# Kernel tuning notes

Hardware: AMD Instinct MI355X
Metric: run time of the kernel (lower is better)

Reference implementation:

```python
import jax, jax.numpy as jnp
import numpy as np

N = 50000       # nodes
E = 800000      # edges (avg degree 16)
H = 64          # hidden_channels
T = 4           # towers
F = H // T      # per-tower channels (divide_input=True) = 16
NAGG, NSC = 5, 3
# degree histogram passed as mol_deg -> avg log-degree scaler constant (as in PyG PNAConv)
MOL_DEG = np.array([0, 5, 15, 30, 25, 15, 7, 2, 1], dtype=np.float64)
_bins = np.arange(len(MOL_DEG))
AVG_LOG = float((np.log(_bins + 1.0) * MOL_DEG).sum() / MOL_DEG.sum())


def setup_inputs() -> dict:
    key = jax.random.key(0)
    ks = jax.random.split(key, 12)
    g = lambda k, shp, s=0.1: jax.random.normal(k, shp, dtype=jnp.float32) * s
    return {
        "atom_x": g(ks[0], (N, H), 1.0),
        "bond_emb": g(ks[1], (5, H)),                      # Embedding(5, H)
        "edge_w": g(ks[2], (H, F)), "edge_b": jnp.zeros((F,), jnp.float32),
        "pre_w1": g(ks[3], (T, 3 * F, F)), "pre_b1": jnp.zeros((T, F), jnp.float32),
        "pre_w2": g(ks[4], (T, F, F)), "pre_b2": jnp.zeros((T, F), jnp.float32),
        "post_w1": g(ks[5], (T, (1 + NAGG * NSC) * F, F)), "post_b1": jnp.zeros((T, F), jnp.float32),
        "post_w2": g(ks[6], (T, F, F)), "post_b2": jnp.zeros((T, F), jnp.float32),
        "lin_w": g(ks[7], (H, H)), "lin_b": jnp.zeros((H,), jnp.float32),
        "ln_g": jnp.ones((H,), jnp.float32), "ln_b": jnp.zeros((H,), jnp.float32),
        "bond_x": jax.random.randint(ks[8], (E,), 0, 5),
        "atom_edge_index": jax.random.randint(ks[9], (2, E), 0, N),
    }


def reference(atom_x, bond_emb, edge_w, edge_b, pre_w1, pre_b1, pre_w2, pre_b2,
              post_w1, post_b1, post_w2, post_b2, lin_w, lin_b, ln_g, ln_b,
              bond_x, atom_edge_index):
    src, dst = atom_edge_index[0], atom_edge_index[1]
    # bond encoder + PNA edge encoder (edge_dim -> F_in)
    e = bond_emb[bond_x] @ edge_w + edge_b                       # [E, F]
    xt = atom_x.reshape(N, T, F)                                 # divide_input
    x_j, x_i = xt[src], xt[dst]                                  # [E, T, F]
    et = jnp.broadcast_to(e[:, None, :], (E, T, F))
    h = jnp.concatenate([x_i, x_j, et], axis=-1)                 # [E, T, 3F]
    # per-tower pre-MLP (Linear -> ReLU -> Linear)
    h = jax.nn.relu(jnp.einsum('etf,tfg->etg', h, pre_w1) + pre_b1)
    h = jnp.einsum('etf,tfg->etg', h, pre_w2) + pre_b2           # messages [E, T, F]

    s = jax.ops.segment_sum(h, dst, num_segments=N)
    cnt = jax.ops.segment_sum(jnp.ones((E,), h.dtype), dst, num_segments=N)
    cnt_c = jnp.maximum(cnt, 1.0)[:, None, None]
    mean = s / cnt_c
    mean2 = jax.ops.segment_sum(h * h, dst, num_segments=N) / cnt_c
    std = jnp.sqrt(jax.nn.relu(mean2 - mean * mean) + 1e-5)
    has = (cnt > 0)[:, None, None]
    mn = jnp.where(has, jax.ops.segment_min(h, dst, num_segments=N), 0.0)
    mx = jnp.where(has, jax.ops.segment_max(h, dst, num_segments=N), 0.0)
    agg = jnp.concatenate([s, mean, mn, mx, std], axis=-1)       # [N, T, 5F]

    # degree scalers (deg clamped to 1, as in PyG DegreeScalerAggregation)
    ld = jnp.log(jnp.maximum(cnt, 1.0) + 1.0)[:, None, None]
    agg = jnp.concatenate([agg, agg * (ld / AVG_LOG), agg * (AVG_LOG / ld)], axis=-1)  # [N, T, 15F]

    out = jnp.concatenate([xt, agg], axis=-1)                    # [N, T, 16F]
    # per-tower post-MLP, then mix towers with final Linear
    out = jax.nn.relu(jnp.einsum('ntf,tfg->ntg', out, post_w1) + post_b1)
    out = jnp.einsum('ntf,tfg->ntg', out, post_w2) + post_b2     # [N, T, F]
    out = out.reshape(N, H) @ lin_w + lin_b                      # [N, H]

    # LayerNorm + ReLU + residual (dropout is identity in eval)
    mu = out.mean(-1, keepdims=True)
    var = out.var(-1, keepdims=True)
    ln = (out - mu) / jnp.sqrt(var + 1e-5) * ln_g + ln_b
    return atom_x + jax.nn.relu(ln)
```

## Files before the change

### kernel.cpp

```cpp
#include <hip/hip_runtime.h>
#include <cstdint>

typedef unsigned short u16;

#define AVG_LOG_F 1.4862356961977451f
#define MAXD 64

#define OFF_W2   3072
#define OFF_PW1  4096
#define OFF_PW2  20480
#define OFF_LW   21504
#define OFF_PB1  25600
#define OFF_PB2  25664
#define OFF_QB1  25728
#define OFF_QB2  25792
#define OFF_LB   25856
#define OFF_LG   25920
#define OFF_LBN  25984
#define OFF_EWT  26128
#define IB       26448

__device__ __forceinline__ float bf2f(u16 u) {
    return __uint_as_float(((unsigned)u) << 16);
}
__device__ __forceinline__ u16 f2bf(float f) {
    unsigned u = __float_as_uint(f);
    u += 0x7fffu + ((u >> 16) & 1u);
    return (u16)(u >> 16);
}
__device__ __forceinline__ float rdin(const void* p, long j, int mode) {
    if (mode == 0) return bf2f(((const u16*)p)[j]);
    return ((const float*)p)[j];
}
template <int MODE>
__device__ __forceinline__ void load16c(const void* p, long base, float* o) {
    if (MODE == 0) {
        const u16* q = (const u16*)p + base;
        uint4 a = *(const uint4*)q;
        uint4 b = *(const uint4*)(q + 8);
        o[0]  = __uint_as_float(a.x << 16); o[1]  = __uint_as_float(a.x & 0xffff0000u);
        o[2]  = __uint_as_float(a.y << 16); o[3]  = __uint_as_float(a.y & 0xffff0000u);
        o[4]  = __uint_as_float(a.z << 16); o[5]  = __uint_as_float(a.z & 0xffff0000u);
        o[6]  = __uint_as_float(a.w << 16); o[7]  = __uint_as_float(a.w & 0xffff0000u);
        o[8]  = __uint_as_float(b.x << 16); o[9]  = __uint_as_float(b.x & 0xffff0000u);
        o[10] = __uint_as_float(b.y << 16); o[11] = __uint_as_float(b.y & 0xffff0000u);
        o[12] = __uint_as_float(b.z << 16); o[13] = __uint_as_float(b.z & 0xffff0000u);
        o[14] = __uint_as_float(b.w << 16); o[15] = __uint_as_float(b.w & 0xffff0000u);
    } else {
        const float* q = (const float*)p + base;
        float4 a = *(const float4*)q;
        float4 b = *(const float4*)(q + 4);
        float4 c = *(const float4*)(q + 8);
        float4 d = *(const float4*)(q + 12);
        o[0]=a.x; o[1]=a.y; o[2]=a.z; o[3]=a.w;
        o[4]=b.x; o[5]=b.y; o[6]=b.z; o[7]=b.w;
        o[8]=c.x; o[9]=c.y; o[10]=c.z; o[11]=c.w;
        o[12]=d.x; o[13]=d.y; o[14]=d.z; o[15]=d.w;
    }
}

template <int MODE>
__device__ __forceinline__ void y_loop(const void* ax, const void* pre_w1, float* wsY, float* wsXW,
                                       int Nn, int wave, int nwaves, int l) {
    const int t = l >> 4, g = l & 15;
    float wxi[16], wxj[16];
#pragma unroll
    for (int f = 0; f < 16; f++) {
        wxi[f] = rdin(pre_w1, t * 768 + f * 16 + g, MODE);
        wxj[f] = rdin(pre_w1, t * 768 + (16 + f) * 16 + g, MODE);
    }
    for (int n = wave; n < Nn; n += nwaves) {
        float xj[16];
        load16c<MODE>(ax, (long)n * 64 + t * 16, xj);
        float accY = 0.f, accX = 0.f;
#pragma unroll
        for (int f = 0; f < 16; f++) {
            accY = fmaf(xj[f], wxj[f], accY);
            accX = fmaf(xj[f], wxi[f], accX);
        }
        wsY[(long)n * 64 + l]  = accY;
        wsXW[(long)n * 64 + l] = accX;
    }
}

__global__ __launch_bounds__(256) void k_prep(
    const int* __restrict__ dstp, const int* __restrict__ srcp, const int* __restrict__ bondp,
    const void* bond_emb, const void* edge_w, const void* edge_b,
    const void* pre_w1, const void* pre_b1, const void* pre_w2, const void* pre_b2,
    const void* post_w1, const void* post_b1, const void* post_w2, const void* post_b2,
    const void* lin_w, const void* lin_b, const void* ln_g, const void* ln_b,
    const void* ax, float* wsf, float* wsY, float* wsXW,
    int* __restrict__ cnt, int* __restrict__ pk, int* modep,
    int Nn, int E, int NIB)
{
    int tid = threadIdx.x;
    if ((int)blockIdx.x >= NIB) {
        int e = ((int)blockIdx.x - NIB) * 256 + tid;
        if (e < E) {
            int d = dstp[e];
            int pos = atomicAdd(&cnt[d], 1);
            if (pos < MAXD) pk[d * MAXD + pos] = (srcp[e] << 9) | (bondp[e] & 7);
        }
        return;
    }
    __shared__ int csh;
    __shared__ float ET[80];
    if (tid == 0) csh = 0;
    __syncthreads();
    {
        unsigned v = ((const unsigned*)ax)[tid];
        unsigned lo = v & 0xffffu;
        int ee = (int)((lo >> 7) & 0xff);
        int isbf = (lo == 0u) || (ee >= 110 && ee <= 140);
        atomicAdd(&csh, isbf);
    }
    __syncthreads();
    int mode = (csh >= 192) ? 0 : 1;

    int b = (int)blockIdx.x;
    int gt = b * 256 + tid;
    int gs = NIB * 256;
    if (b == 0 && tid == 0) modep[0] = mode;

    for (int j = gt; j < 1024; j += gs)  wsf[OFF_W2 + j]  = rdin(pre_w2, j, mode);
    for (int j = gt; j < 16384; j += gs) wsf[OFF_PW1 + j] = rdin(post_w1, j, mode);
    for (int j = gt; j < 1024; j += gs)  wsf[OFF_PW2 + j] = rdin(post_w2, j, mode);
    for (int j = gt; j < 4096; j += gs)  wsf[OFF_LW + j]  = rdin(lin_w, j, mode);
    for (int j = gt; j < 64; j += gs) {
        wsf[OFF_PB1 + j] = rdin(pre_b1, j, mode);
        wsf[OFF_PB2 + j] = rdin(pre_b2, j, mode);
        wsf[OFF_QB1 + j] = rdin(post_b1, j, mode);
        wsf[OFF_QB2 + j] = rdin(post_b2, j, mode);
        wsf[OFF_LB + j]  = rdin(lin_b, j, mode);
        wsf[OFF_LG + j]  = rdin(ln_g, j, mode);
        wsf[OFF_LBN + j] = rdin(ln_b, j, mode);
    }
    if (b == 0) {
        if (tid < 80) {
            int bb = tid >> 4, f = tid & 15;
            float acc = rdin(edge_b, f, mode);
            for (int k = 0; k < 64; k++)
                acc = fmaf(rdin(bond_emb, bb * 64 + k, mode), rdin(edge_w, k * 16 + f, mode), acc);
            ET[tid] = acc;
        }
        __syncthreads();
        for (int j = tid; j < 320; j += 256) {
            int bb = j >> 6, ll = j & 63, tt = ll >> 4, gg = ll & 15;
            float acc = rdin(pre_b1, tt * 16 + gg, mode);
#pragma unroll
            for (int f = 0; f < 16; f++)
                acc = fmaf(ET[bb * 16 + f], rdin(pre_w1, tt * 768 + (32 + f) * 16 + gg, mode), acc);
            wsf[OFF_EWT + j] = acc;
        }
    }
    int wave = gt >> 6;
    int nwaves = gs >> 6;
    int l = tid & 63;
    if (mode == 0) y_loop<0>(ax, pre_w1, wsY, wsXW, Nn, wave, nwaves, l);
    else           y_loop<1>(ax, pre_w1, wsY, wsXW, Nn, wave, nwaves, l);
}

__global__ __launch_bounds__(256, 4) void k_node(
    const void* __restrict__ ax, const float* __restrict__ Yp, const float* __restrict__ XWp,
    const int* __restrict__ pk, const int* __restrict__ cnt,
    const float* __restrict__ wsf, void* __restrict__ outp,
    const int* __restrict__ modep, int Nn)
{
    __shared__ float hb[4][8][64];
    __shared__ float zws[4][5][64];
    __shared__ float qp[4][4][64];
    __shared__ float xrow[4][64];
    __shared__ float scl1s[4], scl2s[4];
    const int w = threadIdx.x >> 6;
    const int l = threadIdx.x & 63;
    const int t = l >> 4;
    const int g = l & 15;
    const int n = blockIdx.x * 4 + w;
    const int mode = modep[0];
    const bool active = (n < Nn);
    const int nn = active ? n : 0;

    const float* W2  = wsf + OFF_W2  + t * 256;
    const float* PW1 = wsf + OFF_PW1 + t * 4096;
    const float* PW2 = wsf + OFF_PW2 + t * 256;

    int probe = __builtin_amdgcn_update_dpp(0, l & 15, 0x121, 0xf, 0xf, false);
    int p0 = __builtin_amdgcn_readfirstlane(probe);
    const int dir = (p0 == 1) ? 1 : -1;

    float w2r[16];
#pragma unroll
    for (int r = 0; r < 16; r++) w2r[r] = W2[((g + dir * r) & 15) * 16 + g];

    float pb2g = wsf[OFF_PB2 + t * 16 + g];
    float qb1g = wsf[OFF_QB1 + t * 16 + g];
    float qb2g = wsf[OFF_QB2 + t * 16 + g];

    int deg = active ? cnt[nn] : 0;
    if (deg > MAXD) deg = MAXD;

    int   pkvAll = pk[nn * MAXD + l];
    float XWv    = XWp[(long)nn * 64 + l];
    zws[w][0][l] = XWv + wsf[OFF_EWT + 0 * 64 + l];
    zws[w][1][l] = XWv + wsf[OFF_EWT + 1 * 64 + l];
    zws[w][2][l] = XWv + wsf[OFF_EWT + 2 * 64 + l];
    zws[w][3][l] = XWv + wsf[OFF_EWT + 3 * 64 + l];
    zws[w][4][l] = XWv + wsf[OFF_EWT + 4 * 64 + l];
    xrow[w][l]   = rdin(ax, (long)nn * 64 + l, mode);

    float s = 0.f, s2 = 0.f, mn = 3.0e38f, mx = -3.0e38f;

#define ROTFMA(r, ctrl)                                                              \
    {                                                                                \
        int tmp_ = __builtin_amdgcn_update_dpp(0, hi, ctrl, 0xf, 0xf, false);        \
        float hv_ = __int_as_float(tmp_);                                            \
        if ((r) & 1) mb = fmaf(hv_, w2r[r], mb);                                     \
        else         ma = fmaf(hv_, w2r[r], ma);                                     \
    }

    for (int kb = 0; kb < deg; kb += 8) {
        float yv[8];
        int   vs[8];
#pragma unroll
        for (int k = 0; k < 8; k++) {
            if (kb + k < deg) {
                vs[k] = __builtin_amdgcn_readlane(pkvAll, kb + k);
                yv[k] = Yp[(vs[k] >> 3) + l];
            }
        }
#pragma unroll
        for (int k = 0; k < 8; k++) {
            if (kb + k < deg) {
                float h = fmaxf(yv[k] + zws[w][vs[k] & 7][l], 0.f);
                int hi = __float_as_uint(h);
                float ma = fmaf(h, w2r[0], pb2g);
                float mb = 0.f;
                ROTFMA(1, 0x121);  ROTFMA(2, 0x122);  ROTFMA(3, 0x123);
                ROTFMA(4, 0x124);  ROTFMA(5, 0x125);  ROTFMA(6, 0x126);
                ROTFMA(7, 0x127);  ROTFMA(8, 0x128);  ROTFMA(9, 0x129);
                ROTFMA(10, 0x12A); ROTFMA(11, 0x12B); ROTFMA(12, 0x12C);
                ROTFMA(13, 0x12D); ROTFMA(14, 0x12E); ROTFMA(15, 0x12F);
                float m = ma + mb;
                s += m;
                s2 = fmaf(m, m, s2);
                mn = fminf(mn, m);
                mx = fmaxf(mx, m);
            }
        }
    }
#undef ROTFMA

    if (deg == 0) { mn = 0.f; mx = 0.f; }
    float cf = (float)(deg > 0 ? deg : 1);
    float inv = 1.0f / cf;
    float mean = s * inv;
    float var = s2 * inv - mean * mean;
    float sd = sqrtf(fmaxf(var, 0.f) + 1e-5f);
    float ldv = logf(cf + 1.0f);
    float sc1 = ldv * (1.0f / AVG_LOG_F);
    float sc2 = AVG_LOG_F / ldv;

    hb[w][0][l] = s;
    hb[w][1][l] = mean;
    hb[w][2][l] = mn;
    hb[w][3][l] = mx;
    hb[w][4][l] = sd;
    if (l == 0) { scl1s[w] = sc1; scl2s[w] = sc2; }
    __syncthreads();

    const int F0 = w * 4;
    float q0[4] = {0,0,0,0}, q1[4] = {0,0,0,0}, q2[4] = {0,0,0,0};
    {
        float xa[4][4];
#pragma unroll
        for (int nd = 0; nd < 4; nd++) {
            float4 v = *(const float4*)&xrow[nd][t * 16 + F0];
            xa[nd][0] = v.x; xa[nd][1] = v.y; xa[nd][2] = v.z; xa[nd][3] = v.w;
        }
#pragma unroll
        for (int fi = 0; fi < 4; fi++) {
            float wv = PW1[(F0 + fi) * 16 + g];
#pragma unroll
            for (int nd = 0; nd < 4; nd++) q0[nd] = fmaf(xa[nd][fi], wv, q0[nd]);
        }
    }
#pragma unroll
    for (int a = 0; a < 5; a++) {
        float xa[4][4];
#pragma unroll
        for (int nd = 0; nd < 4; nd++) {
            float4 v = *(const float4*)&hb[nd][a][t * 16 + F0];
            xa[nd][0] = v.x; xa[nd][1] = v.y; xa[nd][2] = v.z; xa[nd][3] = v.w;
        }
        const int rb = 16 + a * 16;
#pragma unroll
        for (int fi = 0; fi < 4; fi++) {
            const int r = (rb + F0 + fi) * 16 + g;
            float w0  = PW1[r];
            float w1  = PW1[r + 80 * 16];
            float w2v = PW1[r + 160 * 16];
#pragma unroll
            for (int nd = 0; nd < 4; nd++) {
                float x = xa[nd][fi];
                q0[nd] = fmaf(x, w0,  q0[nd]);
                q1[nd] = fmaf(x, w1,  q1[nd]);
                q2[nd] = fmaf(x, w2v, q2[nd]);
            }
        }
    }
#pragma unroll
    for (int nd = 0; nd < 4; nd++)
        qp[w][nd][l] = fmaf(scl2s[nd], q2[nd], fmaf(scl1s[nd], q1[nd], q0[nd]));
    __syncthreads();

    {
        float q0s = qp[0][w][l] + qp[1][w][l] + qp[2][w][l] + qp[3][w][l];
        float p1 = fmaxf(q0s + qb1g, 0.f);
        hb[w][5][l] = p1;
        float pw2c[16];
#pragma unroll
        for (int f = 0; f < 16; f++) pw2c[f] = PW2[f * 16 + g];
        float m2 = qb2g;
        const float4* pp = (const float4*)&hb[w][5][t * 16];
        float4 p0v = pp[0], r1 = pp[1], r2 = pp[2], r3 = pp[3];
        m2 = fmaf(p0v.x, pw2c[0],  m2); m2 = fmaf(p0v.y, pw2c[1],  m2);
        m2 = fmaf(p0v.z, pw2c[2],  m2); m2 = fmaf(p0v.w, pw2c[3],  m2);
        m2 = fmaf(r1.x, pw2c[4],  m2); m2 = fmaf(r1.y, pw2c[5],  m2);
        m2 = fmaf(r1.z, pw2c[6],  m2); m2 = fmaf(r1.w, pw2c[7],  m2);
        m2 = fmaf(r2.x, pw2c[8],  m2); m2 = fmaf(r2.y, pw2c[9],  m2);
        m2 = fmaf(r2.z, pw2c[10], m2); m2 = fmaf(r2.w, pw2c[11], m2);
        m2 = fmaf(r3.x, pw2c[12], m2); m2 = fmaf(r3.y, pw2c[13], m2);
        m2 = fmaf(r3.z, pw2c[14], m2); m2 = fmaf(r3.w, pw2c[15], m2);
        hb[w][6][l] = m2;
    }
    __syncthreads();

    {
        const float* LW = wsf + OFF_LW;
        const int fb = w * 16;
        float lw[4] = {0,0,0,0};
#pragma unroll
        for (int c = 0; c < 4; c++) {
            float pa[4][4];
#pragma unroll
            for (int nd = 0; nd < 4; nd++) {
                float4 v = *(const float4*)&hb[nd][6][fb + 4 * c];
                pa[nd][0] = v.x; pa[nd][1] = v.y; pa[nd][2] = v.z; pa[nd][3] = v.w;
            }
#pragma unroll
            for (int fi = 0; fi < 4; fi++) {
                float wl = LW[(fb + 4 * c + fi) * 64 + l];
#pragma unroll
                for (int nd = 0; nd < 4; nd++) lw[nd] = fmaf(pa[nd][fi], wl, lw[nd]);
            }
        }
#pragma unroll
        for (int nd = 0; nd < 4; nd++) qp[w][nd][l] = lw[nd];
    }
    __syncthreads();

    {
        float a = wsf[OFF_LB + l] + qp[0][w][l] + qp[1][w][l] + qp[2][w][l] + qp[3][w][l];
        float s1 = a, sq = a * a;
#pragma unroll
        for (int o = 1; o < 64; o <<= 1) { s1 += __shfl_xor(s1, o); sq += __shfl_xor(sq, o); }
        float mu = s1 * (1.0f / 64.0f);
        float varl = sq * (1.0f / 64.0f) - mu * mu;
        float ln = (a - mu) * rsqrtf(varl + 1e-5f) * wsf[OFF_LG + l] + wsf[OFF_LBN + l];
        if (active) {
            long idx = (long)n * 64 + l;
            float res = xrow[w][l] + fmaxf(ln, 0.f);
            if (mode == 0) ((u16*)outp)[idx] = f2bf(res);
            else           ((float*)outp)[idx] = res;
        }
    }
}

extern "C" void kernel_launch(void* const* d_in, const int* in_sizes, int n_in,
                              void* d_out, int out_size, void* d_ws, size_t ws_size,
                              hipStream_t stream) {
    const void* atom_x   = d_in[0];
    const void* bond_emb = d_in[1];
    const void* edge_w   = d_in[2];
    const void* edge_b   = d_in[3];
    const void* pre_w1   = d_in[4];
    const void* pre_b1   = d_in[5];
    const void* pre_w2   = d_in[6];
    const void* pre_b2   = d_in[7];
    const void* post_w1  = d_in[8];
    const void* post_b1  = d_in[9];
    const void* post_w2  = d_in[10];
    const void* post_b2  = d_in[11];
    const void* lin_w    = d_in[12];
    const void* lin_b    = d_in[13];
    const void* ln_g     = d_in[14];
    const void* ln_b     = d_in[15];
    const int* bond_x    = (const int*)d_in[16];
    const int* aei       = (const int*)d_in[17];

    int E  = in_sizes[16];
    int Nn = in_sizes[0] / 64;
    const int* srcp = aei;
    const int* dstp = aei + E;

    float* wsf = (float*)d_ws;
    int*   wsi = (int*)d_ws;

    size_t o = IB;
    int* modep = wsi + o; o += 16;
    int* cnt   = wsi + o; o += Nn;
    o = (o + 63) & ~(size_t)63;
    int* pk    = wsi + o; o += (size_t)Nn * MAXD;
    float* Yp  = (float*)(wsi + o); o += (size_t)Nn * 64;
    float* XWp = (float*)(wsi + o); o += (size_t)Nn * 64;

    const int NIB  = 1600;
    const int SBLK = (E + 255) / 256;

    (void)hipMemsetAsync(cnt, 0, (size_t)Nn * sizeof(int), stream);
    k_prep<<<NIB + SBLK, 256, 0, stream>>>(dstp, srcp, bond_x,
                                           bond_emb, edge_w, edge_b,
                                           pre_w1, pre_b1, pre_w2, pre_b2,
                                           post_w1, post_b1, post_w2, post_b2,
                                           lin_w, lin_b, ln_g, ln_b,
                                           atom_x, wsf, Yp, XWp, cnt, pk, modep, Nn, E, NIB);
    dim3 gn((Nn + 3) / 4, 1, 1);
    k_node<<<gn, 256, 0, stream>>>(atom_x, Yp, XWp, pk, cnt, wsf, d_out, modep, Nn);
}
```

Baseline: 298.9 us.

## Compute per-edge pre-MLP second layer with fp16 MFMA over 16-edge batches

Replaces the per-edge DPP-rotation FMA matvec for the second pre-MLP layer with 16x16x16 fp16 MFMA instructions. Each wave stages 16 edges of hidden activations as fp16 in a swizzled shared buffer and multiplies them against per-tower W2 fragments. Per-lane partial statistics are then reduced across lane groups with shuffles. This cuts the VALU/DPP instruction count per edge but adds shared-memory round trips, padding waste for nodes with low degree, and fp16 precision loss.

```diff
diff --git a/kernel.cpp b/kernel.cpp
--- a/kernel.cpp
+++ b/kernel.cpp
@@ -2,6 +2,8 @@
 #include <cstdint>
 
 typedef unsigned short u16;
+typedef _Float16 half4v __attribute__((ext_vector_type(4)));
+typedef float f32x4 __attribute__((ext_vector_type(4)));
 
 #define AVG_LOG_F 1.4862356961977451f
 #define MAXD 64
@@ -167,6 +169,7 @@
     const int* __restrict__ modep, int Nn)
 {
     __shared__ float hb[4][8][64];
+    __shared__ _Float16 hbh[4][16][64];
     __shared__ float zws[4][5][64];
     __shared__ float qp[4][4][64];
     __shared__ float xrow[4][64];
@@ -180,19 +183,23 @@
     const bool active = (n < Nn);
     const int nn = active ? n : 0;
 
-    const float* W2  = wsf + OFF_W2  + t * 256;
     const float* PW1 = wsf + OFF_PW1 + t * 4096;
     const float* PW2 = wsf + OFF_PW2 + t * 256;
 
-    int probe = __builtin_amdgcn_update_dpp(0, l & 15, 0x121, 0xf, 0xf, false);
-    int p0 = __builtin_amdgcn_readfirstlane(probe);
-    const int dir = (p0 == 1) ? 1 : -1;
-
-    float w2r[16];
-#pragma unroll
-    for (int r = 0; r < 16; r++) w2r[r] = W2[((g + dir * r) & 15) * 16 + g];
-
-    float pb2g = wsf[OFF_PB2 + t * 16 + g];
+    half4v bfr[4];
+    float pb2a[4];
+    {
+        const int k4 = (l >> 4) << 2;
+#pragma unroll
+        for (int tt = 0; tt < 4; tt++) {
+            half4v bv;
+#pragma unroll
+            for (int i = 0; i < 4; i++)
+                bv[i] = (_Float16)wsf[OFF_W2 + tt * 256 + (k4 + i) * 16 + (l & 15)];
+            bfr[tt] = bv;
+            pb2a[tt] = wsf[OFF_PB2 + tt * 16 + (l & 15)];
+        }
+    }
     float qb1g = wsf[OFF_QB1 + t * 16 + g];
     float qb2g = wsf[OFF_QB2 + t * 16 + g];
 
@@ -208,47 +215,77 @@
     zws[w][4][l] = XWv + wsf[OFF_EWT + 4 * 64 + l];
     xrow[w][l]   = rdin(ax, (long)nn * 64 + l, mode);
 
-    float s = 0.f, s2 = 0.f, mn = 3.0e38f, mx = -3.0e38f;
-
-#define ROTFMA(r, ctrl)                                                              \
-    {                                                                                \
-        int tmp_ = __builtin_amdgcn_update_dpp(0, hi, ctrl, 0xf, 0xf, false);        \
-        float hv_ = __int_as_float(tmp_);                                            \
-        if ((r) & 1) mb = fmaf(hv_, w2r[r], mb);                                     \
-        else         ma = fmaf(hv_, w2r[r], ma);                                     \
-    }
-
-    for (int kb = 0; kb < deg; kb += 8) {
-        float yv[8];
-        int   vs[8];
-#pragma unroll
-        for (int k = 0; k < 8; k++) {
-            if (kb + k < deg) {
+    float sA[4]  = {0.f, 0.f, 0.f, 0.f};
+    float s2A[4] = {0.f, 0.f, 0.f, 0.f};
+    float mnA[4] = {3.0e38f, 3.0e38f, 3.0e38f, 3.0e38f};
+    float mxA[4] = {-3.0e38f, -3.0e38f, -3.0e38f, -3.0e38f};
+
+    const _Float16* hrow = &hbh[w][l & 15][0];
+    const int swz = (l & 7) << 3;
+    const int aidx0 = (l >> 4) << 2;
+
+    for (int kb = 0; kb < deg; kb += 16) {
+        int B = deg - kb; if (B > 16) B = 16;
+        int vs[16]; float yv[16];
+#pragma unroll
+        for (int k = 0; k < 16; k++) {
+            if (k < B) {
                 vs[k] = __builtin_amdgcn_readlane(pkvAll, kb + k);
                 yv[k] = Yp[(vs[k] >> 3) + l];
             }
         }
 #pragma unroll
-        for (int k = 0; k < 8; k++) {
-            if (kb + k < deg) {
-                float h = fmaxf(yv[k] + zws[w][vs[k] & 7][l], 0.f);
-                int hi = __float_as_uint(h);
-                float ma = fmaf(h, w2r[0], pb2g);
-                float mb = 0.f;
-                ROTFMA(1, 0x121);  ROTFMA(2, 0x122);  ROTFMA(3, 0x123);
-                ROTFMA(4, 0x124);  ROTFMA(5, 0x125);  ROTFMA(6, 0x126);
-                ROTFMA(7, 0x127);  ROTFMA(8, 0x128);  ROTFMA(9, 0x129);
-                ROTFMA(10, 0x12A); ROTFMA(11, 0x12B); ROTFMA(12, 0x12C);
-                ROTFMA(13, 0x12D); ROTFMA(14, 0x12E); ROTFMA(15, 0x12F);
-                float m = ma + mb;
-                s += m;
-                s2 = fmaf(m, m, s2);
-                mn = fminf(mn, m);
-                mx = fmaxf(mx, m);
-            }
-        }
-    }
-#undef ROTFMA
+        for (int k = 0; k < 16; k++) {
+            float hv = (k < B) ? fmaxf(yv[k] + zws[w][vs[k] & 7][l], 0.f) : 0.f;
+            hbh[w][k][l ^ ((k & 7) << 3)] = (_Float16)hv;
+        }
+        if (B == 16) {
+#pragma unroll
+            for (int tt = 0; tt < 4; tt++) {
+                half4v a = *(const half4v*)&hrow[(tt * 16 + aidx0) ^ swz];
+                f32x4 d = __builtin_amdgcn_mfma_f32_16x16x16f16(a, bfr[tt], (f32x4){0.f,0.f,0.f,0.f}, 0, 0, 0);
+#pragma unroll
+                for (int i = 0; i < 4; i++) {
+                    float m = d[i] + pb2a[tt];
+                    sA[tt] += m;
+                    s2A[tt] = fmaf(m, m, s2A[tt]);
+                    mnA[tt] = fminf(mnA[tt], m);
+                    mxA[tt] = fmaxf(mxA[tt], m);
+                }
+            }
+        } else {
+            const int ebase = kb + aidx0;
+#pragma unroll
+            for (int tt = 0; tt < 4; tt++) {
+                half4v a = *(const half4v*)&hrow[(tt * 16 + aidx0) ^ swz];
+                f32x4 d = __builtin_amdgcn_mfma_f32_16x16x16f16(a, bfr[tt], (f32x4){0.f,0.f,0.f,0.f}, 0, 0, 0);
+#pragma unroll
+                for (int i = 0; i < 4; i++) {
+                    bool val = (ebase + i) < deg;
+                    float m = d[i] + pb2a[tt];
+                    float mm = val ? m : 0.f;
+                    sA[tt] += mm;
+                    s2A[tt] = fmaf(mm, mm, s2A[tt]);
+                    mnA[tt] = fminf(mnA[tt], val ? m : 3.0e38f);
+                    mxA[tt] = fmaxf(mxA[tt], val ? m : -3.0e38f);
+                }
+            }
+        }
+    }
+
+#pragma unroll
+    for (int tt = 0; tt < 4; tt++) {
+        sA[tt]  += __shfl_xor(sA[tt], 16);  sA[tt]  += __shfl_xor(sA[tt], 32);
+        s2A[tt] += __shfl_xor(s2A[tt], 16); s2A[tt] += __shfl_xor(s2A[tt], 32);
+        mnA[tt] = fminf(mnA[tt], __shfl_xor(mnA[tt], 16));
+        mnA[tt] = fminf(mnA[tt], __shfl_xor(mnA[tt], 32));
+        mxA[tt] = fmaxf(mxA[tt], __shfl_xor(mxA[tt], 16));
+        mxA[tt] = fmaxf(mxA[tt], __shfl_xor(mxA[tt], 32));
+    }
+    float s  = (t & 2) ? ((t & 1) ? sA[3]  : sA[2])  : ((t & 1) ? sA[1]  : sA[0]);
+    float s2 = (t & 2) ? ((t & 1) ? s2A[3] : s2A[2]) : ((t & 1) ? s2A[1] : s2A[0]);
+    float mn = (t & 2) ? ((t & 1) ? mnA[3] : mnA[2]) : ((t & 1) ? mnA[1] : mnA[0]);
+    float mx = (t & 2) ? ((t & 1) ? mxA[3] : mxA[2]) : ((t & 1) ? mxA[1] : mxA[0]);
 
     if (deg == 0) { mn = 0.f; mx = 0.f; }
     float cf = (float)(deg > 0 ? deg : 1);
```

Result: faster. 289.2 us (-3.3%).
